# Optimization experiments

Measured on AMD Instinct MI355X. Metric: run time of the kernel, lower is better.

Reference implementation:

```python
import jax, jax.numpy as jnp
import numpy as np

B, V, C, H, W = 2, 5, 16, 512, 640
N = 131072


def _bilinear_sample(fm, gx, gy):
    # fm: [BV, C, H, W]; gx, gy: [BV, P] normalized coords in [-1, 1]
    # Replicates F.grid_sample(mode='bilinear', padding_mode='zeros', align_corners=False)
    BV, Cc, Hh, Ww = fm.shape
    ix = ((gx + 1.0) * Ww - 1.0) * 0.5
    iy = ((gy + 1.0) * Hh - 1.0) * 0.5
    x0 = jnp.floor(ix)
    y0 = jnp.floor(iy)
    wx1 = ix - x0
    wy1 = iy - y0
    wx0 = 1.0 - wx1
    wy0 = 1.0 - wy1
    img = fm.reshape(BV, Cc, Hh * Ww)
    out = 0.0
    for xc, yc, w in ((x0, y0, wx0 * wy0), (x0 + 1, y0, wx1 * wy0),
                      (x0, y0 + 1, wx0 * wy1), (x0 + 1, y0 + 1, wx1 * wy1)):
        valid = ((xc >= 0) & (xc <= Ww - 1) & (yc >= 0) & (yc <= Hh - 1))
        xi = jnp.clip(xc, 0, Ww - 1).astype(jnp.int32)
        yi = jnp.clip(yc, 0, Hh - 1).astype(jnp.int32)
        idx = (yi * Ww + xi)[:, None, :]  # [BV,1,P]
        vals = jnp.take_along_axis(img, jnp.broadcast_to(idx, (BV, Cc, idx.shape[-1])), axis=2)
        out = out + vals * (w * valid.astype(fm.dtype))[:, None, :]
    return out  # [BV, C, P]


def setup_inputs() -> dict:
    key = jax.random.key(0)
    k1, k2, k3, k4 = jax.random.split(key, 4)
    feature_maps = jax.random.normal(k1, (B, V, C, H, W), dtype=jnp.float32)
    fx = fy = 500.0
    cx, cy = W / 2.0, H / 2.0
    K = jnp.array([[fx, 0.0, cx], [0.0, fy, cy], [0.0, 0.0, 1.0]], jnp.float32)
    cam_intrinsics = jnp.broadcast_to(K, (B, V, 3, 3)).copy()
    E = jnp.concatenate([jnp.eye(3, dtype=jnp.float32), jnp.zeros((3, 1), jnp.float32)], axis=1)
    cam_extrinsics = jnp.broadcast_to(E, (B, V, 3, 4)).copy()
    # back-project random in-image pixels at random depths -> valid 3D points
    u = jax.random.uniform(k2, (B, N), minval=2.0, maxval=W - 3.0)
    v = jax.random.uniform(k3, (B, N), minval=2.0, maxval=H - 3.0)
    z = jax.random.uniform(k4, (B, N), minval=2.0, maxval=10.0)
    x = (u - cx) / fx * z
    y = (v - cy) / fy * z
    pts = jnp.stack([x, y, z], axis=1)  # [B, 3, N]
    return {"feature_maps": feature_maps, "pts": pts,
            "cam_intrinsics": cam_intrinsics, "cam_extrinsics": cam_extrinsics}


def reference(feature_maps, pts, cam_intrinsics, cam_extrinsics):
    b, v, c, h, w = feature_maps.shape
    bv = b * v
    n = pts.shape[2]
    fm = feature_maps.reshape(bv, c, h, w)
    K = cam_intrinsics.reshape(bv, 3, 3)
    E = cam_extrinsics.reshape(bv, 3, 4)
    pts_e = jnp.broadcast_to(pts[:, None], (b, v, 3, n)).reshape(bv, 3, n)
    # p_cam = R p + t
    tp = jnp.einsum('bij,bjn->bin', E[:, :, :3], pts_e) + E[:, :, 3:4]  # [bv,3,n]
    xx, yy, zz = tp[:, 0], tp[:, 1], tp[:, 2]
    normal_uv = jnp.stack([xx / zz, yy / zz, jnp.ones_like(xx)], axis=-1)  # [bv,n,3]
    uv = jnp.einsum('bnk,bjk->bnj', normal_uv, K)[..., :2]  # [bv,n,2]
    gx = (uv[..., 0] - 0.5) / float(w - 1) * 2.0 - 1.0
    gy = (uv[..., 1] - 0.5) / float(h - 1) * 2.0 - 1.0
    dx = 2.0 / float(w - 1)
    dy = 2.0 / float(h - 1)

    def get_features(gx_, gy_):
        return _bilinear_sample(fm, gx_, gy_).reshape(b, v, c, n)

    f = get_features(gx, gy)
    f_l = get_features(gx - dx, gy)
    f_r = get_features(gx + dx, gy)
    f_t = get_features(gx, gy - dy)
    f_b = get_features(gx, gy + dy)
    grad_x = 0.5 * (f_r - f_l)
    grad_y = 0.5 * (f_b - f_t)
    f_grad = jnp.stack([grad_x, grad_y], axis=-1)  # [b,v,c,n,2]
    return (f, f_grad)
```

## Files before the change

kernel.cpp:

```cpp
#include <hip/hip_runtime.h>


namespace {
constexpr int Bc = 2, Vc = 5, Cc = 16, Hc = 512, Wc = 640;
constexpr int Nc = 131072;
constexpr int BVc = Bc * Vc;
constexpr int HWc = Hc * Wc;
constexpr int CHUNK = 4;
constexpr int NBIN = 128;
constexpr int NBLK = Nc / 256;

constexpr size_t FMT_CH   = (size_t)CHUNK * HWc * Cc * sizeof(float);
constexpr size_t TEMP_CH  = (size_t)CHUNK * Nc * 48 * sizeof(float);
constexpr size_t IDX_B    = (size_t)BVc * Nc * sizeof(int);
constexpr size_t HIST_B   = (size_t)BVc * NBIN * NBLK * sizeof(unsigned);
constexpr size_t TOT_B    = (size_t)BVc * NBIN * sizeof(unsigned);
constexpr size_t OFF_FMT   = 0;
constexpr size_t OFF_TEMP  = OFF_FMT + FMT_CH;
constexpr size_t OFF_IDX   = OFF_TEMP + TEMP_CH;
constexpr size_t OFF_RANK  = OFF_IDX + IDX_B;
constexpr size_t OFF_PACK  = OFF_RANK + IDX_B;
constexpr size_t OFF_HIST  = OFF_PACK + IDX_B;
constexpr size_t OFF_OFFT  = OFF_HIST + HIST_B;
constexpr size_t OFF_TOT   = OFF_OFFT + HIST_B;
constexpr size_t OFF_BASE  = OFF_TOT + TOT_B;
constexpr size_t WS_NEED   = OFF_BASE + TOT_B;

typedef float f32x2 __attribute__((ext_vector_type(2)));
typedef float f32x4 __attribute__((ext_vector_type(4)));

__device__ __forceinline__ void axis_decomp(float t, int limit,
                                            int& i0, int& i1,
                                            float& w0, float& w1) {
    float f0 = floorf(t);
    float fr = t - f0;
    float f1 = f0 + 1.0f;
    float lim = (float)(limit - 1);
    w0 = (1.0f - fr) * ((f0 >= 0.0f && f0 <= lim) ? 1.0f : 0.0f);
    w1 = fr * ((f1 >= 0.0f && f1 <= lim) ? 1.0f : 0.0f);
    int i = (int)f0;
    i0 = min(max(i, 0), limit - 1);
    i1 = min(max(i + 1, 0), limit - 1);
}

__device__ __forceinline__ void project(const float* __restrict__ pts,
                                        const float* __restrict__ Kmat,
                                        const float* __restrict__ Emat,
                                        int bv, int n, float& ix, float& iy) {
    const int b = bv / Vc;
    const float px = pts[(b * 3 + 0) * Nc + n];
    const float py = pts[(b * 3 + 1) * Nc + n];
    const float pz = pts[(b * 3 + 2) * Nc + n];
    const float* E = Emat + bv * 12;
    const float xx = E[0] * px + E[1] * py + E[2]  * pz + E[3];
    const float yy = E[4] * px + E[5] * py + E[6]  * pz + E[7];
    const float zz = E[8] * px + E[9] * py + E[10] * pz + E[11];
    const float* K = Kmat + bv * 9;
    const float inv_z = 1.0f / zz;
    const float nx = xx * inv_z;
    const float ny = yy * inv_z;
    const float u = K[0] * nx + K[1] * ny + K[2];
    const float v = K[3] * nx + K[4] * ny + K[5];
    const float gx = (u - 0.5f) * (2.0f / (float)(Wc - 1)) - 1.0f;
    const float gy = (v - 0.5f) * (2.0f / (float)(Hc - 1)) - 1.0f;
    ix = ((gx + 1.0f) * (float)Wc - 1.0f) * 0.5f;
    iy = ((gy + 1.0f) * (float)Hc - 1.0f) * 0.5f;
}

__global__ __launch_bounds__(256) void hist_kernel(
    const float* __restrict__ pts, const float* __restrict__ Kmat,
    const float* __restrict__ Emat,
    unsigned* __restrict__ histT,
    unsigned* __restrict__ packed) {
    __shared__ unsigned lh[NBIN];
    const int t = (int)threadIdx.x;
    const int blk = (int)blockIdx.x & (NBLK - 1);
    const int bv = (int)blockIdx.x >> 9;
    const int n = (blk << 8) | t;
    if (t < NBIN) lh[t] = 0u;
    __syncthreads();
    float ix, iy;
    project(pts, Kmat, Emat, bv, n, ix, iy);
    const int y0 = min(max((int)floorf(iy), 0), Hc - 1);
    const unsigned bin = (unsigned)(y0 >> 2);
    const unsigned lrank = atomicAdd(&lh[bin], 1u);
    packed[bv * Nc + n] = (bin << 16) | lrank;
    __syncthreads();
    if (t < NBIN) histT[(size_t)((bv * NBIN) + t) * NBLK + blk] = lh[t];
}

__global__ __launch_bounds__(512) void scan_kernel(
    const unsigned* __restrict__ histT, unsigned* __restrict__ offT,
    unsigned* __restrict__ totals) {
    __shared__ unsigned s[NBLK];
    const int row = (int)blockIdx.x;
    const int t = (int)threadIdx.x;
    const unsigned own = histT[(size_t)row * NBLK + t];
    s[t] = own;
    __syncthreads();
#pragma unroll
    for (int off = 1; off < NBLK; off <<= 1) {
        const unsigned v = (t >= off) ? s[t - off] : 0u;
        __syncthreads();
        s[t] += v;
        __syncthreads();
    }
    offT[(size_t)row * NBLK + t] = s[t] - own;
    if (t == NBLK - 1) totals[row] = s[t];
}

__global__ void base_kernel(const unsigned* __restrict__ totals,
                            unsigned* __restrict__ bin_base) {
    const int bv = (int)threadIdx.x;
    if (bv < BVc) {
        unsigned s = 0;
        for (int b2 = 0; b2 < NBIN; ++b2) {
            bin_base[bv * NBIN + b2] = s;
            s += totals[bv * NBIN + b2];
        }
    }
}

__global__ __launch_bounds__(256) void scatter2_kernel(
    const unsigned* __restrict__ packed, const unsigned* __restrict__ offT,
    const unsigned* __restrict__ bin_base,
    int* __restrict__ idx, int* __restrict__ rank) {
    const int t = (int)threadIdx.x;
    const int blk = (int)blockIdx.x & (NBLK - 1);
    const int bv = (int)blockIdx.x >> 9;
    const int n = (blk << 8) | t;
    const unsigned p = packed[bv * Nc + n];
    const unsigned bin = p >> 16;
    const unsigned lrank = p & 0xFFFFu;
    const int row = bv * NBIN + (int)bin;
    const unsigned pos = bin_base[row] + offT[(size_t)row * NBLK + blk] + lrank;
    idx[bv * Nc + (int)pos] = n;
    rank[bv * Nc + n] = (int)pos;
}

__global__ __launch_bounds__(256) void transpose_kernel(
    const float* __restrict__ fm, float* __restrict__ fmt, int bv_base) {
    __shared__ float lds[16 * 256];
    const int blocks_per_bv = HWc / 256;
    const int bvl = (int)blockIdx.x / blocks_per_bv;
    const int bv = bv_base + bvl;
    const int pix0 = ((int)blockIdx.x % blocks_per_bv) * 256;
    const int t = (int)threadIdx.x;
#pragma unroll
    for (int i = 0; i < 4; ++i) {
        const int l = i * 256 + t;
        const int c = l >> 6;
        const int m = l & 63;
        const float4 v = *reinterpret_cast<const float4*>(
            fm + (size_t)(bv * 16 + c) * HWc + pix0 + 4 * m);
        *reinterpret_cast<float4*>(&lds[c * 256 + 4 * m]) = v;
    }
    __syncthreads();
    float4* dst = reinterpret_cast<float4*>(fmt + (size_t)(bvl * HWc + pix0) * 16);
#pragma unroll
    for (int j = 0; j < 4; ++j) {
        const int q = j * 256 + t;
        const int p = q >> 2;
        const int k = q & 3;
        float4 v;
        v.x = lds[(4 * k + 0) * 256 + p];
        v.y = lds[(4 * k + 1) * 256 + p];
        v.z = lds[(4 * k + 2) * 256 + p];
        v.w = lds[(4 * k + 3) * 256 + p];
        dst[q] = v;
    }
}

__global__ __launch_bounds__(256) void gather_sorted_kernel(
    const float* __restrict__ fmt,
    const float* __restrict__ pts,
    const float* __restrict__ Kmat,
    const float* __restrict__ Emat,
    const int* __restrict__ idx,
    float* __restrict__ temp,
    int bv_base) {
    __shared__ float lds[256 * 48];
    const int t = (int)threadIdx.x;
    const int bvl = (int)blockIdx.x >> 9;
    const int B = (int)blockIdx.x & 511;
    const int j = ((B & 7) << 6) | (B >> 3);
    const int pos = (j << 8) | t;
    const int bv = bv_base + bvl;
    const int n = idx[bv * Nc + pos];
    const int b = bv / Vc;

    const float px = pts[(b * 3 + 0) * Nc + n];
    const float py = pts[(b * 3 + 1) * Nc + n];
    const float pz = pts[(b * 3 + 2) * Nc + n];
    const float* E = Emat + bv * 12;
    const float xx = E[0] * px + E[1] * py + E[2]  * pz + E[3];
    const float yy = E[4] * px + E[5] * py + E[6]  * pz + E[7];
    const float zz = E[8] * px + E[9] * py + E[10] * pz + E[11];
    const float* K = Kmat + bv * 9;
    const float inv_z = 1.0f / zz;
    const float nx = xx * inv_z;
    const float ny = yy * inv_z;
    const float u = K[0] * nx + K[1] * ny + K[2];
    const float v = K[3] * nx + K[4] * ny + K[5];
    const float gx = (u - 0.5f) * (2.0f / (float)(Wc - 1)) - 1.0f;
    const float gy = (v - 0.5f) * (2.0f / (float)(Hc - 1)) - 1.0f;
    const float ix = ((gx + 1.0f) * (float)Wc - 1.0f) * 0.5f;
    const float iy = ((gy + 1.0f) * (float)Hc - 1.0f) * 0.5f;
    const float sx = (float)Wc / (float)(Wc - 1);
    const float sy = (float)Hc / (float)(Hc - 1);

    int xc0, xc1, xl0, xl1, xr0, xr1;
    int yc0, yc1, yt0, yt1, yb0, yb1;
    float wxc0, wxc1, wxl0, wxl1, wxr0, wxr1;
    float wyc0, wyc1, wyt0, wyt1, wyb0, wyb1;
    axis_decomp(ix,      Wc, xc0, xc1, wxc0, wxc1);
    axis_decomp(ix - sx, Wc, xl0, xl1, wxl0, wxl1);
    axis_decomp(ix + sx, Wc, xr0, xr1, wxr0, wxr1);
    axis_decomp(iy,      Hc, yc0, yc1, wyc0, wyc1);
    axis_decomp(iy - sy, Hc, yt0, yt1, wyt0, wyt1);
    axis_decomp(iy + sy, Hc, yb0, yb1, wyb0, wyb1);

    float4 accF[4], accGx[4], accGy[4];
#pragma unroll
    for (int q = 0; q < 4; ++q) {
        accF[q]  = make_float4(0.f, 0.f, 0.f, 0.f);
        accGx[q] = make_float4(0.f, 0.f, 0.f, 0.f);
        accGy[q] = make_float4(0.f, 0.f, 0.f, 0.f);
    }

    const float* plane = fmt + (size_t)bvl * HWc * 16;

    auto tap = [&](int x, int y, float w, float4* acc) {
        const float4* p = reinterpret_cast<const float4*>(plane + (size_t)(y * Wc + x) * 16);
#pragma unroll
        for (int q = 0; q < 4; ++q) {
            float4 vv = p[q];
            acc[q].x += w * vv.x;
            acc[q].y += w * vv.y;
            acc[q].z += w * vv.z;
            acc[q].w += w * vv.w;
        }
    };
    auto sample = [&](int x0, int x1, float wx0, float wx1,
                      int y0, int y1, float wy0, float wy1,
                      float4* acc, float s) {
        tap(x0, y0, s * wx0 * wy0, acc);
        tap(x1, y0, s * wx1 * wy0, acc);
        tap(x0, y1, s * wx0 * wy1, acc);
        tap(x1, y1, s * wx1 * wy1, acc);
    };

    sample(xc0, xc1, wxc0, wxc1, yc0, yc1, wyc0, wyc1, accF,  1.0f);
    sample(xl0, xl1, wxl0, wxl1, yc0, yc1, wyc0, wyc1, accGx, -0.5f);
    sample(xr0, xr1, wxr0, wxr1, yc0, yc1, wyc0, wyc1, accGx,  0.5f);
    sample(xc0, xc1, wxc0, wxc1, yt0, yt1, wyt0, wyt1, accGy, -0.5f);
    sample(xc0, xc1, wxc0, wxc1, yb0, yb1, wyb0, wyb1, accGy,  0.5f);

    float* lb = lds + t * 48;
#pragma unroll
    for (int q = 0; q < 4; ++q) {
        const float fs[4]  = {accF[q].x,  accF[q].y,  accF[q].z,  accF[q].w};
        const float gxs[4] = {accGx[q].x, accGx[q].y, accGx[q].z, accGx[q].w};
        const float gys[4] = {accGy[q].x, accGy[q].y, accGy[q].z, accGy[q].w};
#pragma unroll
        for (int k = 0; k < 4; ++k) {
            const int c = 4 * q + k;
            lb[c]           = fs[k];
            lb[16 + 2 * c]  = gxs[k];
            lb[17 + 2 * c]  = gys[k];
        }
    }
    __syncthreads();
    const f32x4* l4 = reinterpret_cast<const f32x4*>(lds);
    f32x4* t4 = reinterpret_cast<f32x4*>(temp) + (size_t)(bvl * Nc + (j << 8)) * 12;
#pragma unroll
    for (int i = 0; i < 12; ++i) {
        __builtin_nontemporal_store(l4[i * 256 + t], t4 + i * 256 + t);
    }
}

__global__ __launch_bounds__(256) void unpermute_kernel(
    const float* __restrict__ temp, const int* __restrict__ rank,
    float* __restrict__ out_f, float* __restrict__ out_g, int bv_base) {
    __shared__ float lds[48 * 260];
    const int t = (int)threadIdx.x;
    const int bvl = (int)blockIdx.x >> 9;
    const int n0 = ((int)blockIdx.x & 511) << 8;
    const int bv = bv_base + bvl;
    const int n = n0 + t;
    const int pos = rank[bv * Nc + n];
    const f32x4* t4 = reinterpret_cast<const f32x4*>(temp) + (size_t)(bvl * Nc + pos) * 12;
#pragma unroll
    for (int q = 0; q < 12; ++q) {
        f32x4 v = __builtin_nontemporal_load(t4 + q);
        lds[(4 * q + 0) * 260 + t] = v.x;
        lds[(4 * q + 1) * 260 + t] = v.y;
        lds[(4 * q + 2) * 260 + t] = v.z;
        lds[(4 * q + 3) * 260 + t] = v.w;
    }
    __syncthreads();
#pragma unroll
    for (int c = 0; c < 16; ++c) {
        __builtin_nontemporal_store(lds[c * 260 + t],
                                    out_f + (size_t)(bv * 16 + c) * Nc + n);
        f32x2 g2 = {lds[(16 + 2 * c) * 260 + t], lds[(17 + 2 * c) * 260 + t]};
        __builtin_nontemporal_store(g2, reinterpret_cast<f32x2*>(out_g) +
                                            (size_t)(bv * 16 + c) * Nc + n);
    }
}

__device__ __forceinline__ float bilin(const float* __restrict__ base,
                                       int x0, int x1, float wx0, float wx1,
                                       int y0, int y1, float wy0, float wy1) {
    const float* r0 = base + y0 * Wc;
    const float* r1 = base + y1 * Wc;
    return wy0 * (wx0 * r0[x0] + wx1 * r0[x1]) +
           wy1 * (wx0 * r1[x0] + wx1 * r1[x1]);
}

__global__ __launch_bounds__(256) void fgf_fallback_kernel(
    const float* __restrict__ fm, const float* __restrict__ pts,
    const float* __restrict__ Kmat, const float* __restrict__ Emat,
    float* __restrict__ out_f, float* __restrict__ out_g) {
    const int n   = (((int)blockIdx.x & 511) << 8) | (int)threadIdx.x;
    const int bvc = (int)blockIdx.x >> 9;
    const int bv  = bvc >> 4;
    float ix, iy;
    project(pts, Kmat, Emat, bv, n, ix, iy);
    const float sx = (float)Wc / (float)(Wc - 1);
    const float sy = (float)Hc / (float)(Hc - 1);

    int xc0, xc1, xl0, xl1, xr0, xr1, yc0, yc1, yt0, yt1, yb0, yb1;
    float wxc0, wxc1, wxl0, wxl1, wxr0, wxr1, wyc0, wyc1, wyt0, wyt1, wyb0, wyb1;
    axis_decomp(ix,      Wc, xc0, xc1, wxc0, wxc1);
    axis_decomp(ix - sx, Wc, xl0, xl1, wxl0, wxl1);
    axis_decomp(ix + sx, Wc, xr0, xr1, wxr0, wxr1);
    axis_decomp(iy,      Hc, yc0, yc1, wyc0, wyc1);
    axis_decomp(iy - sy, Hc, yt0, yt1, wyt0, wyt1);
    axis_decomp(iy + sy, Hc, yb0, yb1, wyb0, wyb1);

    const float* base = fm + (size_t)bvc * HWc;
    const float fc = bilin(base, xc0, xc1, wxc0, wxc1, yc0, yc1, wyc0, wyc1);
    const float fl = bilin(base, xl0, xl1, wxl0, wxl1, yc0, yc1, wyc0, wyc1);
    const float fr = bilin(base, xr0, xr1, wxr0, wxr1, yc0, yc1, wyc0, wyc1);
    const float ft = bilin(base, xc0, xc1, wxc0, wxc1, yt0, yt1, wyt0, wyt1);
    const float fb = bilin(base, xc0, xc1, wxc0, wxc1, yb0, yb1, wyb0, wyb1);

    const size_t out_idx = (size_t)blockIdx.x * 256 + threadIdx.x;
    out_f[out_idx] = fc;
    *reinterpret_cast<float2*>(out_g + out_idx * 2) =
        make_float2(0.5f * (fr - fl), 0.5f * (fb - ft));
}

}

extern "C" void kernel_launch(void* const* d_in, const int* in_sizes, int n_in,
                              void* d_out, int out_size, void* d_ws, size_t ws_size,
                              hipStream_t stream) {
    const float* fm  = (const float*)d_in[0];
    const float* pts = (const float*)d_in[1];
    const float* K   = (const float*)d_in[2];
    const float* E   = (const float*)d_in[3];
    float* out_f = (float*)d_out;
    float* out_g = out_f + (size_t)BVc * Cc * Nc;

    if (ws_size >= WS_NEED) {
        char* ws = (char*)d_ws;
        float*    fmt      = (float*)(ws + OFF_FMT);
        float*    temp     = (float*)(ws + OFF_TEMP);
        int*      idx      = (int*)(ws + OFF_IDX);
        int*      rank     = (int*)(ws + OFF_RANK);
        unsigned* packed   = (unsigned*)(ws + OFF_PACK);
        unsigned* histT    = (unsigned*)(ws + OFF_HIST);
        unsigned* offT     = (unsigned*)(ws + OFF_OFFT);
        unsigned* totals   = (unsigned*)(ws + OFF_TOT);
        unsigned* bin_base = (unsigned*)(ws + OFF_BASE);

        hist_kernel<<<BVc * NBLK, 256, 0, stream>>>(pts, K, E, histT, packed);
        scan_kernel<<<BVc * NBIN, NBLK, 0, stream>>>(histT, offT, totals);
        base_kernel<<<1, 64, 0, stream>>>(totals, bin_base);
        scatter2_kernel<<<BVc * NBLK, 256, 0, stream>>>(packed, offT, bin_base, idx, rank);

        for (int g = 0; g < BVc; g += CHUNK) {
            const int cs = min(CHUNK, BVc - g);
            transpose_kernel<<<cs * (HWc / 256), 256, 0, stream>>>(fm, fmt, g);
            gather_sorted_kernel<<<cs * (Nc / 256), 256, 0, stream>>>(
                fmt, pts, K, E, idx, temp, g);
            unpermute_kernel<<<cs * (Nc / 256), 256, 0, stream>>>(
                temp, rank, out_f, out_g, g);
        }
    } else {
        fgf_fallback_kernel<<<BVc * Cc * (Nc / 256), 256, 0, stream>>>(
            fm, pts, K, E, out_f, out_g);
    }
}
```

Measured before the change: 818.8 us.

## Split gather work across four threads per point by channel group

The sorted gather kernel now assigns four threads per point, each handling a 4-channel group, instead of one thread handling all 16 channels. This cuts per-thread registers and allows direct vectorized stores of each thread's slice of the 48-float record, removing the LDS staging buffer and the __syncthreads. The trade-off is that the projection and axis decomposition are recomputed four times per point, and four times as many blocks are launched.

```diff
diff --git a/kernel.cpp b/kernel.cpp
--- a/kernel.cpp
+++ b/kernel.cpp
@@ -179,12 +179,12 @@
     const int* __restrict__ idx,
     float* __restrict__ temp,
     int bv_base) {
-    __shared__ float lds[256 * 48];
-    const int t = (int)threadIdx.x;
-    const int bvl = (int)blockIdx.x >> 9;
-    const int B = (int)blockIdx.x & 511;
-    const int j = ((B & 7) << 6) | (B >> 3);
-    const int pos = (j << 8) | t;
+    const int t = (int)threadIdx.x;
+    const int cg = t & 3;
+    const int bvl = (int)blockIdx.x >> 11;
+    const int B = (int)blockIdx.x & 2047;
+    const int j = ((B & 7) << 8) | (B >> 3);
+    const int pos = (j << 6) | (t >> 2);
     const int bv = bv_base + bvl;
     const int n = idx[bv * Nc + pos];
     const int b = bv / Vc;
@@ -220,30 +220,23 @@
     axis_decomp(iy - sy, Hc, yt0, yt1, wyt0, wyt1);
     axis_decomp(iy + sy, Hc, yb0, yb1, wyb0, wyb1);
 
-    float4 accF[4], accGx[4], accGy[4];
-#pragma unroll
-    for (int q = 0; q < 4; ++q) {
-        accF[q]  = make_float4(0.f, 0.f, 0.f, 0.f);
-        accGx[q] = make_float4(0.f, 0.f, 0.f, 0.f);
-        accGy[q] = make_float4(0.f, 0.f, 0.f, 0.f);
-    }
-
-    const float* plane = fmt + (size_t)bvl * HWc * 16;
-
-    auto tap = [&](int x, int y, float w, float4* acc) {
-        const float4* p = reinterpret_cast<const float4*>(plane + (size_t)(y * Wc + x) * 16);
-#pragma unroll
-        for (int q = 0; q < 4; ++q) {
-            float4 vv = p[q];
-            acc[q].x += w * vv.x;
-            acc[q].y += w * vv.y;
-            acc[q].z += w * vv.z;
-            acc[q].w += w * vv.w;
-        }
+    float4 accF  = make_float4(0.f, 0.f, 0.f, 0.f);
+    float4 accGx = make_float4(0.f, 0.f, 0.f, 0.f);
+    float4 accGy = make_float4(0.f, 0.f, 0.f, 0.f);
+
+    const float* plane = fmt + (size_t)bvl * HWc * 16 + 4 * cg;
+
+    auto tap = [&](int x, int y, float w, float4& acc) {
+        const float4 vv = *reinterpret_cast<const float4*>(
+            plane + (size_t)(y * Wc + x) * 16);
+        acc.x += w * vv.x;
+        acc.y += w * vv.y;
+        acc.z += w * vv.z;
+        acc.w += w * vv.w;
     };
     auto sample = [&](int x0, int x1, float wx0, float wx1,
                       int y0, int y1, float wy0, float wy1,
-                      float4* acc, float s) {
+                      float4& acc, float s) {
         tap(x0, y0, s * wx0 * wy0, acc);
         tap(x1, y0, s * wx1 * wy0, acc);
         tap(x0, y1, s * wx0 * wy1, acc);
@@ -256,27 +249,13 @@
     sample(xc0, xc1, wxc0, wxc1, yt0, yt1, wyt0, wyt1, accGy, -0.5f);
     sample(xc0, xc1, wxc0, wxc1, yb0, yb1, wyb0, wyb1, accGy,  0.5f);
 
-    float* lb = lds + t * 48;
-#pragma unroll
-    for (int q = 0; q < 4; ++q) {
-        const float fs[4]  = {accF[q].x,  accF[q].y,  accF[q].z,  accF[q].w};
-        const float gxs[4] = {accGx[q].x, accGx[q].y, accGx[q].z, accGx[q].w};
-        const float gys[4] = {accGy[q].x, accGy[q].y, accGy[q].z, accGy[q].w};
-#pragma unroll
-        for (int k = 0; k < 4; ++k) {
-            const int c = 4 * q + k;
-            lb[c]           = fs[k];
-            lb[16 + 2 * c]  = gxs[k];
-            lb[17 + 2 * c]  = gys[k];
-        }
-    }
-    __syncthreads();
-    const f32x4* l4 = reinterpret_cast<const f32x4*>(lds);
-    f32x4* t4 = reinterpret_cast<f32x4*>(temp) + (size_t)(bvl * Nc + (j << 8)) * 12;
-#pragma unroll
-    for (int i = 0; i < 12; ++i) {
-        __builtin_nontemporal_store(l4[i * 256 + t], t4 + i * 256 + t);
-    }
+    float* rec = temp + (size_t)(bvl * Nc + pos) * 48;
+    f32x4 fv = {accF.x, accF.y, accF.z, accF.w};
+    __builtin_nontemporal_store(fv, reinterpret_cast<f32x4*>(rec + 4 * cg));
+    f32x4 g0 = {accGx.x, accGy.x, accGx.y, accGy.y};
+    f32x4 g1 = {accGx.z, accGy.z, accGx.w, accGy.w};
+    __builtin_nontemporal_store(g0, reinterpret_cast<f32x4*>(rec + 16 + 8 * cg));
+    __builtin_nontemporal_store(g1, reinterpret_cast<f32x4*>(rec + 20 + 8 * cg));
 }
 
 __global__ __launch_bounds__(256) void unpermute_kernel(
@@ -384,7 +363,7 @@
         for (int g = 0; g < BVc; g += CHUNK) {
             const int cs = min(CHUNK, BVc - g);
             transpose_kernel<<<cs * (HWc / 256), 256, 0, stream>>>(fm, fmt, g);
-            gather_sorted_kernel<<<cs * (Nc / 256), 256, 0, stream>>>(
+            gather_sorted_kernel<<<cs * (Nc / 64), 256, 0, stream>>>(
                 fmt, pts, K, E, idx, temp, g);
             unpermute_kernel<<<cs * (Nc / 256), 256, 0, stream>>>(
                 temp, rank, out_f, out_g, g);
```

New measurement: 744.7 us. -9.0%, faster.
